# Optimization experiments

Hardware: AMD Instinct MI355X
Metric: run time of the kernel (lower is better)

Reference implementation:

```python
import jax, jax.numpy as jnp
import numpy as np

B, N, D_IN = 2, 2048, 256
H, DH = 8, 32  # num_heads, head_dim (out_features=256, concat=True)


def setup_inputs() -> dict:
    key = jax.random.key(0)
    ks = jax.random.split(key, 7)
    s = 1.0 / np.sqrt(D_IN)
    x = jax.random.normal(ks[0], (B, N, D_IN), dtype=jnp.float32)
    adj = jax.random.randint(ks[1], (B, N, N), 0, 2).astype(jnp.float32)
    eye = jnp.eye(N, dtype=jnp.float32)[None]
    adj = jnp.maximum(adj, eye)
    Wq = jax.random.normal(ks[2], (H * DH, D_IN), dtype=jnp.float32) * s
    Wk = jax.random.normal(ks[3], (H * DH, D_IN), dtype=jnp.float32) * s
    Wv = jax.random.normal(ks[4], (H * DH, D_IN), dtype=jnp.float32) * s
    Wo = jax.random.normal(ks[5], (H * DH, H * DH), dtype=jnp.float32) * s
    bo = jnp.zeros((H * DH,), dtype=jnp.float32)
    return {"x": x, "adj": adj, "Wq": Wq, "Wk": Wk, "Wv": Wv, "Wo": Wo, "bo": bo}


def reference(x, adj, Wq, Wk, Wv, Wo, bo):
    b, n, _ = x.shape
    # projections -> (b, h, n, dh)
    Q = (x @ Wq.T).reshape(b, n, H, DH).transpose(0, 2, 1, 3)
    K = (x @ Wk.T).reshape(b, n, H, DH).transpose(0, 2, 1, 3)
    V = (x @ Wv.T).reshape(b, n, H, DH).transpose(0, 2, 1, 3)
    scores = jnp.einsum('bhnd,bhmd->bhnm', Q, K) / jnp.sqrt(jnp.float32(DH))
    mask = (adj[:, None, :, :] == 0)  # (b,1,n,n) broadcast over heads
    scores = jnp.where(mask, -jnp.inf, scores)
    attn = jax.nn.softmax(scores, axis=-1)  # dropout is identity in eval
    out = jnp.einsum('bhnm,bhmd->bhnd', attn, V)
    out = out.transpose(0, 2, 1, 3).reshape(b, n, H * DH)  # concat heads
    return out @ Wo.T + bo
```

## Files before the change

### kernel.cpp

```cpp
#include <hip/hip_runtime.h>
#include <hip/hip_bf16.h>

#define BB   2
#define NNN  2048
#define DIN  256
#define HH   8
#define DHD  32
#define NW   32

typedef __attribute__((ext_vector_type(8))) short short8;
typedef __attribute__((ext_vector_type(4))) float f32x4;
typedef __attribute__((ext_vector_type(16))) float f32x16;

#if __has_builtin(__builtin_amdgcn_exp2f)
#define EXP2(x) __builtin_amdgcn_exp2f(x)
#else
#define EXP2(x) exp2f(x)
#endif

__device__ __forceinline__ unsigned int pk2(float a, float b) {
  union { __hip_bfloat162 h2; unsigned int u; } cv;
  cv.h2 = __float22bfloat162_rn(float2{a, b});
  return cv.u;
}
__device__ __forceinline__ unsigned short f2bf(float f) {
  unsigned int u = __float_as_uint(f);
  u += 0x7fffu + ((u >> 16) & 1u);
  return (unsigned short)(u >> 16);
}

#define QSCALE (0.17677669529663687f * 1.4426950408889634f)

__global__ __launch_bounds__(256) void prep(
    const float* __restrict__ adj, unsigned long long* __restrict__ Mk,
    const float* __restrict__ x, const float* __restrict__ Wq,
    const float* __restrict__ Wk, const float* __restrict__ Wv,
    unsigned short* __restrict__ Qb, unsigned short* __restrict__ Kb,
    unsigned short* __restrict__ Vt,
    const float* __restrict__ Wo, unsigned short* __restrict__ Wob) {
  __shared__ __align__(16) unsigned short Wl[32][264];
  const int bid = blockIdx.x, tid = threadIdx.x;
  const int w = tid >> 6, lane = tid & 63;

  if (bid >= 2560) {
    int i = (bid - 2560) * 1024 + tid * 4;
    float4 v = *(const float4*)(Wo + i);
    unsigned int p[2] = {pk2(v.x, v.y), pk2(v.z, v.w)};
    *(uint2*)(Wob + i) = *(const uint2*)p;
    return;
  }

  const int grp = bid / 5, rem = bid % 5;
  if (rem < 2) {
    const int mtask = grp * 2 + rem;
    const int row = mtask * 4 + w;
    const float* rp = adj + (size_t)row * NNN + lane * 4;
    float4 vv[8];
    #pragma unroll
    for (int G = 0; G < 8; ++G)
      vv[G] = *(const float4*)(rp + G * 256);
    #pragma unroll
    for (int G = 0; G < 8; ++G) {
      unsigned long long b0 = __ballot(vv[G].x != 0.0f);
      unsigned long long b1 = __ballot(vv[G].y != 0.0f);
      unsigned long long b2 = __ballot(vv[G].z != 0.0f);
      unsigned long long b3 = __ballot(vv[G].w != 0.0f);
      if (lane < 4) {
        unsigned long long bs = (lane == 0) ? b0 : (lane == 1) ? b1 : (lane == 2) ? b2 : b3;
        Mk[(size_t)row * NW + G * 4 + lane] = bs;
      }
    }
  } else {
    const int t = grp * 3 + (rem - 2);
    const int y = t >> 6, rb = t & 63;
    const int mat = y >> 3, ocb = (y & 7) * 32;
    const float* Wsrc = ((mat == 0) ? Wq : (mat == 1) ? Wk : Wv) + (size_t)ocb * DIN;

    #pragma unroll
    for (int it = 0; it < 8; ++it) {
      int f4 = it * 256 + tid;
      int oc = f4 >> 6, k4 = f4 & 63;
      float4 v = *(const float4*)(Wsrc + (size_t)oc * DIN + k4 * 4);
      unsigned int p[2] = {pk2(v.x, v.y), pk2(v.z, v.w)};
      *(uint2*)&Wl[oc][k4 * 4] = *(const uint2*)p;
    }
    __syncthreads();

    const int col = lane & 15, quad = lane >> 4;
    const int row0 = rb * 64 + w * 16;

    f32x4 acc[2];
    #pragma unroll
    for (int c = 0; c < 2; ++c) acc[c] = (f32x4){0.f, 0.f, 0.f, 0.f};

    #pragma unroll
    for (int kk = 0; kk < 8; ++kk) {
      const float* xp = x + (size_t)(row0 + col) * DIN + kk * 32 + quad * 8;
      float4 a0 = *(const float4*)xp, a1 = *(const float4*)(xp + 4);
      union { short8 s; unsigned int u[4]; } af;
      af.u[0] = pk2(a0.x, a0.y); af.u[1] = pk2(a0.z, a0.w);
      af.u[2] = pk2(a1.x, a1.y); af.u[3] = pk2(a1.z, a1.w);
      #pragma unroll
      for (int c = 0; c < 2; ++c) {
        short8 bw = *(const short8*)&Wl[c * 16 + col][kk * 32 + quad * 8];
        acc[c] = __builtin_amdgcn_mfma_f32_16x16x32_bf16(af.s, bw, acc[c], 0, 0, 0);
      }
    }
    const float scale = (mat == 0) ? QSCALE : 1.0f;
    #pragma unroll
    for (int c = 0; c < 2; ++c) {
      int oc = ocb + c * 16 + col, h = oc >> 5, dh = oc & 31;
      #pragma unroll
      for (int r = 0; r < 4; ++r) {
        int row = row0 + quad * 4 + r;
        int b = row >> 11, n = row & (NNN - 1);
        unsigned short val = f2bf(acc[c][r] * scale);
        if (mat == 2)       Vt[((size_t)(b * HH + h) * DHD + dh) * NNN + n] = val;
        else if (mat == 0)  Qb[((size_t)(b * HH + h) * NNN + n) * DHD + dh] = val;
        else                Kb[((size_t)(b * HH + h) * NNN + n) * DHD + dh] = val;
      }
    }
  }
}

__global__ __launch_bounds__(512, 4) void attn(
    const unsigned short* __restrict__ Qb, const unsigned short* __restrict__ Kb,
    const unsigned short* __restrict__ Vt, const unsigned long long* __restrict__ Mk,
    unsigned short* __restrict__ AOb) {
  __shared__ float OL[8][32][33];
  __shared__ float LL[8][32];
  const int tid = threadIdx.x;
  const int w = tid >> 6, lane = tid & 63;
  const int qi = lane & 31, hi = lane >> 5;
  const int bid = blockIdx.x;
  const int xcd = bid & 7, j = bid >> 3;
  const int bh = xcd * 2 + (j >> 6);
  const int qt = j & 63;
  const int b = bh >> 3, h = bh & 7;
  const int q = qt * 32 + qi;
  const int k0 = w * 256;
  const int kq = (qi & ~12) | ((qi & 4) << 1) | ((qi & 8) >> 1);

  const unsigned short* qp = Qb + ((size_t)bh * NNN + q) * DHD + hi * 8;
  const short8 bq0 = *(const short8*)qp;
  const short8 bq1 = *(const short8*)(qp + 16);

  f32x16 accA, accB;
  #pragma unroll
  for (int i = 0; i < 16; ++i) { accA[i] = 0.f; accB[i] = 0.f; }
  float lsum = 0.f;

  const unsigned long long* mrow = Mk + ((size_t)b * NNN + q) * NW + w * 4;
  unsigned int mlo[4], mhi2[4];
  #pragma unroll
  for (int c = 0; c < 4; ++c) {
    unsigned long long mh = mrow[c] >> (2 * hi);
    mlo[c]  = (unsigned int)mh;
    mhi2[c] = (unsigned int)(mh >> 32);
  }

  const unsigned short* kbase = Kb + ((size_t)bh * NNN + k0 + kq) * DHD + hi * 8;
  const unsigned short* vbase = Vt + ((size_t)bh * DHD + qi) * NNN + k0 + hi * 8;

  short8 ak0 = *(const short8*)(kbase);
  short8 ak1 = *(const short8*)(kbase + 16);
  short8 av0 = *(const short8*)(vbase);
  short8 av1 = *(const short8*)(vbase + 16);

  #pragma unroll
  for (int sub = 0; sub < 8; ++sub) {
    const short8 cak0 = ak0, cak1 = ak1, cav0 = av0, cav1 = av1;
    if (sub < 7) {
      const int kn = (sub + 1) * 32;
      ak0 = *(const short8*)(kbase + (size_t)kn * DHD);
      ak1 = *(const short8*)(kbase + (size_t)kn * DHD + 16);
      av0 = *(const short8*)(vbase + kn);
      av1 = *(const short8*)(vbase + kn + 16);
    }

    f32x16 z;
    #pragma unroll
    for (int i = 0; i < 16; ++i) z[i] = 0.f;
    f32x16 st = __builtin_amdgcn_mfma_f32_32x32x16_bf16(cak0, bq0, z, 0, 0, 0);
    st = __builtin_amdgcn_mfma_f32_32x32x16_bf16(cak1, bq1, st, 0, 0, 0);

    unsigned int pk[4][2];
    float gs[4];
    #pragma unroll
    for (int g = 0; g < 4; ++g) {
      const int gofs = (g & 1) + 4 * (g >> 1);
      float pv[4];
      #pragma unroll
      for (int r = 0; r < 4; ++r) {
        unsigned int mwd = (sub < 4) ? mlo[r] : mhi2[r];
        const int pos = (sub & 3) * 8 + gofs;
        int msk = ((int)(mwd << (31 - pos))) >> 31;
        float e = EXP2(st[g * 4 + r]);
        pv[r] = __uint_as_float(__float_as_uint(e) & (unsigned int)msk);
      }
      gs[g] = (pv[0] + pv[1]) + (pv[2] + pv[3]);
      pk[g][0] = pk2(pv[0], pv[1]);
      pk[g][1] = pk2(pv[2], pv[3]);
    }
    lsum += (gs[0] + gs[1]) + (gs[2] + gs[3]);

    union { short8 s; unsigned int u[4]; } F1, F2;
    F1.u[0] = pk[0][0]; F1.u[1] = pk[0][1]; F1.u[2] = pk[1][0]; F1.u[3] = pk[1][1];
    F2.u[0] = pk[2][0]; F2.u[1] = pk[2][1]; F2.u[2] = pk[3][0]; F2.u[3] = pk[3][1];

    accA = __builtin_amdgcn_mfma_f32_32x32x16_bf16(cav0, F1.s, accA, 0, 0, 0);
    accB = __builtin_amdgcn_mfma_f32_32x32x16_bf16(cav1, F2.s, accB, 0, 0, 0);
  }

  lsum += __shfl_xor(lsum, 32, 64);

  #pragma unroll
  for (int g = 0; g < 4; ++g)
    #pragma unroll
    for (int r = 0; r < 4; ++r)
      OL[w][qi][g * 8 + hi * 4 + r] = accA[g * 4 + r] + accB[g * 4 + r];
  if (hi == 0) LL[w][qi] = lsum;
  __syncthreads();

  const int ql = tid >> 4, c2 = (tid & 15) * 2;
  float l = 0.f, o0 = 0.f, o1 = 0.f;
  #pragma unroll
  for (int ww = 0; ww < 8; ++ww) {
    l  += LL[ww][ql];
    o0 += OL[ww][ql][c2];
    o1 += OL[ww][ql][c2 + 1];
  }
  float inv = 1.0f / l;
  unsigned int pr = pk2(o0 * inv, o1 * inv);
  *(unsigned int*)(AOb + ((size_t)(b * NNN + qt * 32 + ql)) * DIN + h * DHD + c2) = pr;
}

__global__ __launch_bounds__(256) void out_proj(const unsigned short* __restrict__ AOb,
                                                const unsigned short* __restrict__ Wob,
                                                const float* __restrict__ bo,
                                                float* __restrict__ out) {
  const int tid = threadIdx.x;
  const int lane = tid & 63, col = lane & 15, quad = lane >> 4;
  const int task = blockIdx.x * 4 + (tid >> 6);
  const int row0 = (task >> 2) * 16;
  const int ocb = (task & 3) * 64;

  f32x4 acc[4];
  #pragma unroll
  for (int c = 0; c < 4; ++c) acc[c] = (f32x4){0.f, 0.f, 0.f, 0.f};

  #pragma unroll
  for (int kk = 0; kk < 8; ++kk) {
    short8 af = *(const short8*)(AOb + (size_t)(row0 + col) * DIN + kk * 32 + quad * 8);
    #pragma unroll
    for (int c = 0; c < 4; ++c) {
      short8 bw = *(const short8*)(Wob + (size_t)(ocb + c * 16 + col) * DIN + kk * 32 + quad * 8);
      acc[c] = __builtin_amdgcn_mfma_f32_16x16x32_bf16(af, bw, acc[c], 0, 0, 0);
    }
  }
  #pragma unroll
  for (int c = 0; c < 4; ++c) {
    int oc = ocb + c * 16 + col;
    float bias = bo[oc];
    #pragma unroll
    for (int r = 0; r < 4; ++r)
      out[(size_t)(row0 + quad * 4 + r) * DIN + oc] = acc[c][r] + bias;
  }
}

extern "C" void kernel_launch(void* const* d_in, const int* in_sizes, int n_in,
                              void* d_out, int out_size, void* d_ws, size_t ws_size,
                              hipStream_t stream) {
  const float* x   = (const float*)d_in[0];
  const float* adj = (const float*)d_in[1];
  const float* Wq  = (const float*)d_in[2];
  const float* Wk  = (const float*)d_in[3];
  const float* Wv  = (const float*)d_in[4];
  const float* Wo  = (const float*)d_in[5];
  const float* bo  = (const float*)d_in[6];
  float* out = (float*)d_out;

  char* ws = (char*)d_ws;
  unsigned short* Qb  = (unsigned short*)(ws);
  unsigned short* Kb  = (unsigned short*)(ws + (2ull << 20));
  unsigned short* Vt  = (unsigned short*)(ws + (4ull << 20));
  unsigned long long* Mk = (unsigned long long*)(ws + (6ull << 20));
  unsigned short* Wob = (unsigned short*)(ws + (7ull << 20));
  unsigned short* AOb = (unsigned short*)(ws + (8ull << 20));

  prep<<<dim3(2624), 256, 0, stream>>>(adj, Mk, x, Wq, Wk, Wv, Qb, Kb, Vt, Wo, Wob);
  attn<<<dim3(1024), 512, 0, stream>>>(Qb, Kb, Vt, Mk, AOb);
  out_proj<<<dim3(256), 256, 0, stream>>>(AOb, Wob, bo, out);
}
```

Before: 151.9 us.

## Cut attention kernel register use to raise occupancy to six blocks per SM

```diff
diff --git a/kernel.cpp b/kernel.cpp
--- a/kernel.cpp
+++ b/kernel.cpp
@@ -123,7 +123,7 @@
   }
 }
 
-__global__ __launch_bounds__(512, 4) void attn(
+__global__ __launch_bounds__(512, 6) void attn(
     const unsigned short* __restrict__ Qb, const unsigned short* __restrict__ Kb,
     const unsigned short* __restrict__ Vt, const unsigned long long* __restrict__ Mk,
     unsigned short* __restrict__ AOb) {
@@ -145,9 +145,9 @@
   const short8 bq0 = *(const short8*)qp;
   const short8 bq1 = *(const short8*)(qp + 16);
 
-  f32x16 accA, accB;
-  #pragma unroll
-  for (int i = 0; i < 16; ++i) { accA[i] = 0.f; accB[i] = 0.f; }
+  f32x16 accO;
+  #pragma unroll
+  for (int i = 0; i < 16; ++i) accO[i] = 0.f;
   float lsum = 0.f;
 
   const unsigned long long* mrow = Mk + ((size_t)b * NNN + q) * NW + w * 4;
@@ -162,27 +162,19 @@
   const unsigned short* kbase = Kb + ((size_t)bh * NNN + k0 + kq) * DHD + hi * 8;
   const unsigned short* vbase = Vt + ((size_t)bh * DHD + qi) * NNN + k0 + hi * 8;
 
-  short8 ak0 = *(const short8*)(kbase);
-  short8 ak1 = *(const short8*)(kbase + 16);
-  short8 av0 = *(const short8*)(vbase);
-  short8 av1 = *(const short8*)(vbase + 16);
-
   #pragma unroll
   for (int sub = 0; sub < 8; ++sub) {
-    const short8 cak0 = ak0, cak1 = ak1, cav0 = av0, cav1 = av1;
-    if (sub < 7) {
-      const int kn = (sub + 1) * 32;
-      ak0 = *(const short8*)(kbase + (size_t)kn * DHD);
-      ak1 = *(const short8*)(kbase + (size_t)kn * DHD + 16);
-      av0 = *(const short8*)(vbase + kn);
-      av1 = *(const short8*)(vbase + kn + 16);
-    }
+    const int kb = sub * 32;
+    short8 ak0 = *(const short8*)(kbase + (size_t)kb * DHD);
+    short8 ak1 = *(const short8*)(kbase + (size_t)kb * DHD + 16);
+    short8 av0 = *(const short8*)(vbase + kb);
+    short8 av1 = *(const short8*)(vbase + kb + 16);
 
     f32x16 z;
     #pragma unroll
     for (int i = 0; i < 16; ++i) z[i] = 0.f;
-    f32x16 st = __builtin_amdgcn_mfma_f32_32x32x16_bf16(cak0, bq0, z, 0, 0, 0);
-    st = __builtin_amdgcn_mfma_f32_32x32x16_bf16(cak1, bq1, st, 0, 0, 0);
+    f32x16 st = __builtin_amdgcn_mfma_f32_32x32x16_bf16(ak0, bq0, z, 0, 0, 0);
+    st = __builtin_amdgcn_mfma_f32_32x32x16_bf16(ak1, bq1, st, 0, 0, 0);
 
     unsigned int pk[4][2];
     float gs[4];
@@ -208,8 +200,8 @@
     F1.u[0] = pk[0][0]; F1.u[1] = pk[0][1]; F1.u[2] = pk[1][0]; F1.u[3] = pk[1][1];
     F2.u[0] = pk[2][0]; F2.u[1] = pk[2][1]; F2.u[2] = pk[3][0]; F2.u[3] = pk[3][1];
 
-    accA = __builtin_amdgcn_mfma_f32_32x32x16_bf16(cav0, F1.s, accA, 0, 0, 0);
-    accB = __builtin_amdgcn_mfma_f32_32x32x16_bf16(cav1, F2.s, accB, 0, 0, 0);
+    accO = __builtin_amdgcn_mfma_f32_32x32x16_bf16(av0, F1.s, accO, 0, 0, 0);
+    accO = __builtin_amdgcn_mfma_f32_32x32x16_bf16(av1, F2.s, accO, 0, 0, 0);
   }
 
   lsum += __shfl_xor(lsum, 32, 64);
@@ -218,7 +210,7 @@
   for (int g = 0; g < 4; ++g)
     #pragma unroll
     for (int r = 0; r < 4; ++r)
-      OL[w][qi][g * 8 + hi * 4 + r] = accA[g * 4 + r] + accB[g * 4 + r];
+      OL[w][qi][g * 8 + hi * 4 + r] = accO[g * 4 + r];
   if (hi == 0) LL[w][qi] = lsum;
   __syncthreads();
 
```

Result: slower. 184.6 us (+21.5%).
